# Kernel tuning notes

Hardware: AMD Instinct MI355X
Metric: run time of the kernel (lower is better)

## Reference

```python
import jax, jax.numpy as jnp
import numpy as np

FS, STRIDE, PAD = 3, 1, 1

def setup_inputs() -> dict:
    key = jax.random.key(0)
    k1, k2, k3 = jax.random.split(key, 3)
    N, C, H, W = 4, 256, 64, 64
    out_C = 256
    x = jax.random.normal(k1, (N, C, H, W), jnp.float32)
    # offset/mask conv params (original inits to 0 -> degenerate; use small random)
    offset_w = jax.random.normal(k2, (FS * FS * 3, C, FS, FS), jnp.float32) * 0.01
    offset_b = jnp.zeros((FS * FS * 3,), jnp.float32)
    # xavier_normal-like scale for dcn weight
    dcn_w = jax.random.normal(k3, (out_C, C, FS, FS), jnp.float32) * (1.0 / np.sqrt(C * FS * FS))
    return {"x": x, "offset_w": offset_w, "offset_b": offset_b, "dcn_w": dcn_w}

def _dcnv2(x, offset_w, offset_b, dcn_w):
    fs, stride, pad = FS, STRIDE, PAD
    N, C, H, W = x.shape
    out_C = dcn_w.shape[0]
    K2 = fs * fs
    om = jax.lax.conv_general_dilated(
        x, offset_w, (stride, stride), [(pad, pad), (pad, pad)],
        dimension_numbers=("NCHW", "OIHW", "NCHW")) + offset_b[None, :, None, None]
    Ho, Wo = om.shape[2], om.shape[3]
    offset = om[:, : 2 * K2].reshape(N, K2, 2, Ho, Wo)
    off_y, off_x = offset[:, :, 0], offset[:, :, 1]            # [N,K2,Ho,Wo]
    mask = jax.nn.sigmoid(om[:, 2 * K2:])                      # [N,K2,Ho,Wo]
    # base sampling grid: ori + kernel tap offset
    ky, kx = jnp.meshgrid(jnp.arange(fs), jnp.arange(fs), indexing="ij")
    ky = ky.reshape(K2).astype(jnp.float32)
    kx = kx.reshape(K2).astype(jnp.float32)
    base_y = (jnp.arange(Ho, dtype=jnp.float32) * stride - pad)[None, :, None] + ky[:, None, None]
    base_x = (jnp.arange(Wo, dtype=jnp.float32) * stride - pad)[None, None, :] + kx[:, None, None]
    h_im = base_y[None] + off_y                                # [N,K2,Ho,Wo]
    w_im = base_x[None] + off_x
    y0 = jnp.floor(h_im)
    x0 = jnp.floor(w_im)
    lh, lw = h_im - y0, w_im - x0
    xf = x.reshape(N, C, H * W)

    def gather(yi, xi):
        valid = (yi >= 0) & (yi <= H - 1) & (xi >= 0) & (xi <= W - 1)
        yc = jnp.clip(yi, 0, H - 1).astype(jnp.int32)
        xc = jnp.clip(xi, 0, W - 1).astype(jnp.int32)
        idx = (yc * W + xc).reshape(N, -1)
        v = jax.vmap(lambda img, ind: img[:, ind])(xf, idx)    # [N,C,K2*Ho*Wo]
        v = v.reshape(N, C, K2, Ho, Wo)
        return v * valid[:, None].astype(x.dtype)

    hh, hw = 1.0 - lh, 1.0 - lw
    sampled = ((hh * hw)[:, None] * gather(y0, x0)
               + (hh * lw)[:, None] * gather(y0, x0 + 1)
               + (lh * hw)[:, None] * gather(y0 + 1, x0)
               + (lh * lw)[:, None] * gather(y0 + 1, x0 + 1))  # [N,C,K2,Ho,Wo]
    sampled = sampled * mask[:, None]
    wk = dcn_w.reshape(out_C, C, K2)
    return jnp.einsum("nckhw,ock->nohw", sampled, wk)

def reference(x, offset_w, offset_b, dcn_w):
    return _dcnv2(x, offset_w, offset_b, dcn_w)
```

## Files before the change

### kernel.cpp

```cpp
#include <hip/hip_runtime.h>
#include <hip/hip_bf16.h>
#include <math.h>

#define NB     4
#define CIN    256
#define HH     64
#define WW     64
#define OUTC   256
#define K2     9
#define KTOT   2304
#define HWSZ   4096
#define NSTEPS 72
#define MTOT   16384


typedef __attribute__((ext_vector_type(4)))  float  floatx4;
typedef __attribute__((ext_vector_type(16))) float  floatx16;
typedef __attribute__((ext_vector_type(8)))  short  short8;
typedef __attribute__((ext_vector_type(4)))  short  short4v;
typedef __attribute__((ext_vector_type(4)))  int    intx4;

__device__ __forceinline__ unsigned short f2bf(float f) {
  union { float f; unsigned u; } v; v.f = f;
  unsigned r = v.u + 0x7FFF + ((v.u >> 16) & 1);
  return (unsigned short)(r >> 16);
}
__device__ __forceinline__ float b2f(unsigned short s) {
  union { unsigned u; float f; } v; v.u = ((unsigned)s) << 16;
  return v.f;
}

#define LDS_BARRIER() asm volatile("s_waitcnt lgkmcnt(0)\n\ts_barrier" ::: "memory")

#define WSM_BFRAG   0
#define WSM_B2FRAG  1179648
#define WSM_XT      (1179648 + 147456)
#define WSM_END     (WSM_XT + NB * HWSZ * CIN * 2)
#define WSF_BW      0
#define WSF_B2W     (KTOT * OUTC * 2)
#define WSF_OM      (WSF_B2W + KTOT * 32 * 2)
#define WSF_END     (WSF_OM + NB * 27 * HWSZ * 4)

__global__ __launch_bounds__(256) void prep_main_kernel(
    const float* __restrict__ dcn_w, const float* __restrict__ offw,
    const float* __restrict__ x,
    unsigned short* __restrict__ Bfrag, unsigned short* __restrict__ B2frag,
    unsigned short* __restrict__ xt) {
  int bid = blockIdx.x;
  int tid = threadIdx.x;
  if (bid < 256) {
    __shared__ unsigned short T[64 * 266];
    int img = bid >> 6, h = bid & 63;
    const float* xp = x + (size_t)img * CIN * HWSZ + h * 64;
    int w = tid & 63, cq = tid >> 6;
    for (int cb = 0; cb < 256; cb += 4) {
      int c = cb + cq;
      T[w * 266 + c] = f2bf(xp[(size_t)c * HWSZ + w]);
    }
    __syncthreads();
    int w2 = tid >> 2, cg = (tid & 3) << 6;
    unsigned short* o = xt + ((size_t)(img * 64 + h) * 64 + w2) * 256 + cg;
#pragma unroll
    for (int i = 0; i < 64; i += 8) {
      short8 v = *(short8*)&T[w2 * 266 + cg + i];
      *(short8*)(o + i) = v;
    }
  } else if (bid < 544) {
    int e = (bid - 256) * 256 + tid;
    int lane = e & 63, nt = (e >> 6) & 7, s16 = e >> 9;
    int n = nt * 32 + (lane & 31);
    int kb = s16 * 16 + ((lane >> 5) << 3);
    short8 pk;
#pragma unroll
    for (int j = 0; j < 8; ++j) {
      int k = kb + j;
      pk[j] = (short)f2bf(dcn_w[n * KTOT + (k & 255) * 9 + (k >> 8)]);
    }
    *(short8*)(Bfrag + (size_t)e * 8) = pk;
  } else {
    int e = (bid - 544) * 256 + tid;
    int lane = e & 63, nt = (e >> 6) & 1, s32 = e >> 7;
    int n = nt * 16 + (lane & 15);
    int kb = s32 * 32 + ((lane >> 4) << 3);
    short8 pk;
#pragma unroll
    for (int j = 0; j < 8; ++j) {
      int k = kb + j;
      pk[j] = (n < 27) ? (short)f2bf(offw[n * KTOT + (k & 255) * 9 + (k >> 8)])
                       : (short)0;
    }
    *(short8*)(B2frag + (size_t)e * 8) = pk;
  }
}

__global__ __launch_bounds__(512, 2) void dcn_fused_kernel(
    const unsigned short* __restrict__ xt,
    const unsigned short* __restrict__ Bfrag,
    const unsigned short* __restrict__ B2frag,
    const float* __restrict__ ob, float* __restrict__ out) {
  __shared__ unsigned short Ald[2][520 * 8];
  __shared__ intx4  sOff[576];
  __shared__ float4 sWt[576];
  __shared__ float  omp[4 * 32 * 68];

  int bid = blockIdx.x;
  int img = bid >> 6, h = bid & 63;
  const unsigned short* xb = xt + (size_t)img * HWSZ * 256;

  int tid  = threadIdx.x;
  int lane = tid & 63, q = tid >> 6;
  int quad = lane >> 4, l15 = lane & 15;
  int l31  = lane & 31,  lh5 = lane >> 5;

  if (q < 4) {
    floatx4 cacc[4][2];
#pragma unroll
    for (int mt = 0; mt < 4; ++mt)
#pragma unroll
      for (int nt = 0; nt < 2; ++nt) cacc[mt][nt] = (floatx4){0.f, 0.f, 0.f, 0.f};
    short8 cpa[2][4];
    short8 cpb[2][2];

#define CONV_LOAD(I, SLOT)                                                     \
  {                                                                            \
    int s = q + (I) * 4;                                                       \
    int t = s >> 3;                                                            \
    int dy = t / 3 - 1, dx = t % 3 - 1;                                        \
    int y = h + dy;                                                            \
    int cb0 = ((s & 7) << 5) + (quad << 3);                                    \
    _Pragma("unroll")                                                          \
    for (int mt = 0; mt < 4; ++mt) {                                           \
      int xx = mt * 16 + l15 + dx;                                             \
      short8 v = {0, 0, 0, 0, 0, 0, 0, 0};                                     \
      if (((unsigned)y < 64u) && ((unsigned)xx < 64u))                         \
        v = *(const short8*)(xb + ((y * 64 + xx) << 8) + cb0);                 \
      cpa[SLOT][mt] = v;                                                       \
    }                                                                          \
    _Pragma("unroll")                                                          \
    for (int nt = 0; nt < 2; ++nt)                                             \
      cpb[SLOT][nt] = *(const short8*)(B2frag + (((s * 2 + nt) * 64 + lane) << 3)); \
  }

    CONV_LOAD(0, 0);
#pragma unroll 2
    for (int i = 0; i < 18; ++i) {
      int sl = i & 1;
      if (i < 17) CONV_LOAD(i + 1, sl ^ 1);
#pragma unroll
      for (int mt = 0; mt < 4; ++mt)
#pragma unroll
        for (int nt = 0; nt < 2; ++nt)
          cacc[mt][nt] = __builtin_amdgcn_mfma_f32_16x16x32_bf16(
              cpa[sl][mt], cpb[sl][nt], cacc[mt][nt], 0, 0, 0);
    }
#undef CONV_LOAD
#pragma unroll
    for (int mt = 0; mt < 4; ++mt)
#pragma unroll
      for (int nt = 0; nt < 2; ++nt) {
        int oc = nt * 16 + l15;
        float4 vv = make_float4(cacc[mt][nt][0], cacc[mt][nt][1],
                                cacc[mt][nt][2], cacc[mt][nt][3]);
        *(float4*)&omp[(q * 32 + oc) * 68 + mt * 16 + quad * 4] = vv;
      }
  }
  __syncthreads();

  for (int v = tid; v < 576; v += 512) {
    int w = v & 63, t = v >> 6;
    int ky = t / 3, kx = t % 3;
    float offy = omp[(0 * 32 + 2 * t) * 68 + w] + omp[(1 * 32 + 2 * t) * 68 + w] +
                 omp[(2 * 32 + 2 * t) * 68 + w] + omp[(3 * 32 + 2 * t) * 68 + w] +
                 ob[2 * t];
    float offx = omp[(0 * 32 + 2 * t + 1) * 68 + w] + omp[(1 * 32 + 2 * t + 1) * 68 + w] +
                 omp[(2 * 32 + 2 * t + 1) * 68 + w] + omp[(3 * 32 + 2 * t + 1) * 68 + w] +
                 ob[2 * t + 1];
    float mraw = omp[(0 * 32 + 18 + t) * 68 + w] + omp[(1 * 32 + 18 + t) * 68 + w] +
                 omp[(2 * 32 + 18 + t) * 68 + w] + omp[(3 * 32 + 18 + t) * 68 + w] +
                 ob[18 + t];
    float mv   = 1.0f / (1.0f + __expf(-mraw));
    float him  = (float)(h - 1 + ky) + offy;
    float wim  = (float)(w - 1 + kx) + offx;
    float y0f = floorf(him), x0f = floorf(wim);
    float lhf = him - y0f, lwf = wim - x0f;
    int y0 = (int)y0f, x0i = (int)x0f;
    bool vy0 = (y0 >= 0) && (y0 < HH);
    bool vy1 = (y0 + 1 >= 0) && (y0 + 1 < HH);
    bool vx0 = (x0i >= 0) && (x0i < WW);
    bool vx1 = (x0i + 1 >= 0) && (x0i + 1 < WW);
    float hh_ = 1.0f - lhf, hw_ = 1.0f - lwf;
    float4 wt;
    wt.x = (vy0 && vx0) ? hh_ * hw_ * mv : 0.0f;
    wt.y = (vy0 && vx1) ? hh_ * lwf * mv : 0.0f;
    wt.z = (vy1 && vx0) ? lhf * hw_ * mv : 0.0f;
    wt.w = (vy1 && vx1) ? lhf * lwf * mv : 0.0f;
    int y0c = min(max(y0, 0), 63), y1c = min(max(y0 + 1, 0), 63);
    int x0c = min(max(x0i, 0), 63), x1c = min(max(x0i + 1, 0), 63);
    intx4 ii = {(y0c * 64 + x0c) << 8, (y0c * 64 + x1c) << 8,
                (y1c * 64 + x0c) << 8, (y1c * 64 + x1c) << 8};
    sOff[v] = ii;
    sWt[v]  = wt;
  }

  floatx16 acc[2];
#pragma unroll
  for (int mt = 0; mt < 2; ++mt)
#pragma unroll
    for (int e = 0; e < 16; ++e) acc[mt][e] = 0.f;

  int sm  = tid >> 3;
  int chk = tid & 7;
  int wgran = (((chk >> 1) << 1) + (sm >> 5)) * 65 + ((chk & 1) << 5) + (sm & 31);

  short8 bfr[2][4];
  short8 cr[4];
  float4 pwt;

  __syncthreads();

#pragma unroll
  for (int sub = 0; sub < 4; ++sub)
    bfr[0][sub] = *(const short8*)(
        Bfrag + (((size_t)sub * 8 + q) * 64 + lane) * 8);
  {
    intx4 off = sOff[sm];
    float4 w0 = sWt[sm];
    int cb = chk * 8;
    cr[0] = *(const short8*)(xb + off.x + cb);
    cr[1] = *(const short8*)(xb + off.y + cb);
    cr[2] = *(const short8*)(xb + off.z + cb);
    cr[3] = *(const short8*)(xb + off.w + cb);
    short8 pk;
#pragma unroll
    for (int j = 0; j < 8; ++j) {
      float v = w0.x * b2f((unsigned short)cr[0][j]) +
                w0.y * b2f((unsigned short)cr[1][j]) +
                w0.z * b2f((unsigned short)cr[2][j]) +
                w0.w * b2f((unsigned short)cr[3][j]);
      pk[j] = (short)f2bf(v);
    }
    *(short8*)&Ald[0][wgran * 8] = pk;
  }
  {
    intx4 off = sOff[sm];
    pwt = sWt[sm];
    int cb = 64 + chk * 8;
    cr[0] = *(const short8*)(xb + off.x + cb);
    cr[1] = *(const short8*)(xb + off.y + cb);
    cr[2] = *(const short8*)(xb + off.z + cb);
    cr[3] = *(const short8*)(xb + off.w + cb);
  }
  LDS_BARRIER();

#pragma unroll 2
  for (int s = 0; s < 36; ++s) {
    int cur = s & 1;
    if (s < 35) {
      int s16b = (s + 1) * 4;
#pragma unroll
      for (int sub = 0; sub < 4; ++sub)
        bfr[cur ^ 1][sub] = *(const short8*)(
            Bfrag + (((size_t)(s16b + sub) * 8 + q) * 64 + lane) * 8);
      short8 pk;
#pragma unroll
      for (int j = 0; j < 8; ++j) {
        float v = pwt.x * b2f((unsigned short)cr[0][j]) +
                  pwt.y * b2f((unsigned short)cr[1][j]) +
                  pwt.z * b2f((unsigned short)cr[2][j]) +
                  pwt.w * b2f((unsigned short)cr[3][j]);
        pk[j] = (short)f2bf(v);
      }
      *(short8*)&Ald[cur ^ 1][wgran * 8] = pk;
    }
    if (s < 34) {
      int s2 = s + 2;
      int t2 = s2 >> 2;
      intx4 off = sOff[t2 * 64 + sm];
      pwt = sWt[t2 * 64 + sm];
      int cb = (s2 & 3) * 64 + chk * 8;
      cr[0] = *(const short8*)(xb + off.x + cb);
      cr[1] = *(const short8*)(xb + off.y + cb);
      cr[2] = *(const short8*)(xb + off.z + cb);
      cr[3] = *(const short8*)(xb + off.w + cb);
    }
#pragma unroll
    for (int sub = 0; sub < 4; ++sub) {
      short8 a0 = *(short8*)&Ald[cur][((sub * 2 + 0) * 65 + lane) * 8];
      short8 a1 = *(short8*)&Ald[cur][((sub * 2 + 1) * 65 + lane) * 8];
      acc[0] = __builtin_amdgcn_mfma_f32_32x32x16_bf16(
          a0, bfr[cur][sub], acc[0], 0, 0, 0);
      acc[1] = __builtin_amdgcn_mfma_f32_32x32x16_bf16(
          a1, bfr[cur][sub], acc[1], 0, 0, 0);
    }
    LDS_BARRIER();
  }

  int oc = q * 32 + l31;
#pragma unroll
  for (int mt = 0; mt < 2; ++mt) {
    float* obase = out + (((size_t)img * OUTC + oc) << 12) + h * 64 +
                   mt * 32 + lh5 * 4;
#pragma unroll
    for (int rg = 0; rg < 4; ++rg) {
      float4 vv = make_float4(acc[mt][rg * 4 + 0], acc[mt][rg * 4 + 1],
                              acc[mt][rg * 4 + 2], acc[mt][rg * 4 + 3]);
      *(float4*)(obase + rg * 8) = vv;
    }
  }
}

__global__ __launch_bounds__(256) void prep_fb_kernel(
    const float* __restrict__ dcn_w, const float* __restrict__ offw,
    unsigned short* __restrict__ Bw, unsigned short* __restrict__ B2w) {
  int oc = blockIdx.x;
  for (int k = threadIdx.x; k < KTOT; k += 256) {
    int t = k >> 8, c = k & 255;
    Bw[oc * KTOT + k] = f2bf(dcn_w[oc * KTOT + c * 9 + t]);
    if (oc < 32)
      B2w[oc * KTOT + k] = (oc < 27) ? f2bf(offw[oc * KTOT + c * 9 + t])
                                     : (unsigned short)0;
  }
}

__global__ __launch_bounds__(256) void conv_offset_kernel(
    const float* __restrict__ x, const unsigned short* __restrict__ B2w,
    const float* __restrict__ ob, float* __restrict__ om) {
  __shared__ unsigned short A_lds[64 * 40];
  __shared__ unsigned short B_lds[32 * 40];
  int bid = blockIdx.x;
  int n = bid >> 6, h = bid & 63;
  int tid = threadIdx.x, lane = tid & 63, q = tid >> 6;
  const float* xn = x + n * (CIN * HWSZ);
  floatx4 acc0 = {0.f, 0.f, 0.f, 0.f}, acc1 = {0.f, 0.f, 0.f, 0.f};
  int w = tid & 63, cg = tid >> 6, ocb = tid >> 3, part = tid & 7;
  for (int s = 0; s < NSTEPS; ++s) {
    int t = s >> 3, c0 = (s & 7) << 5;
    int dy = t / 3 - 1, dx = t % 3 - 1;
    __syncthreads();
    {
      int y = h + dy, xx = w + dx;
      bool inb = ((unsigned)y < 64u) && ((unsigned)xx < 64u);
      const float* xb = xn + (c0 + cg * 8) * HWSZ + y * 64 + xx;
      short8 pk;
#pragma unroll
      for (int j = 0; j < 8; ++j) { float v = inb ? xb[j * HWSZ] : 0.0f; pk[j] = (short)f2bf(v); }
      *(short8*)&A_lds[w * 40 + cg * 8] = pk;
    }
    { const unsigned short* bp = B2w + ocb * KTOT + (t << 8) + c0 + part * 4;
      *(short4v*)&B_lds[ocb * 40 + part * 4] = *(const short4v*)bp; }
    __syncthreads();
    int fr = (lane >> 4) * 8;
    short8 af  = *(short8*)&A_lds[(q * 16 + (lane & 15)) * 40 + fr];
    short8 bf0 = *(short8*)&B_lds[((lane & 15)) * 40 + fr];
    short8 bf1 = *(short8*)&B_lds[(16 + (lane & 15)) * 40 + fr];
    acc0 = __builtin_amdgcn_mfma_f32_16x16x32_bf16(af, bf0, acc0, 0, 0, 0);
    acc1 = __builtin_amdgcn_mfma_f32_16x16x32_bf16(af, bf1, acc1, 0, 0, 0);
  }
  int g = lane >> 4;
#pragma unroll
  for (int nt = 0; nt < 2; ++nt) {
    floatx4 a = nt ? acc1 : acc0;
    int oc = nt * 16 + (lane & 15);
    if (oc < 27) {
      float bias = ob[oc];
#pragma unroll
      for (int r = 0; r < 4; ++r) {
        int wm = q * 16 + g * 4 + r;
        float val = a[r] + bias;
        if (oc >= 18) val = 1.0f / (1.0f + __expf(-val));
        om[((n * 27 + oc) << 12) + h * 64 + wm] = val;
      }
    }
  }
}

__global__ __launch_bounds__(256) void dcn_main_kernel(
    const float* __restrict__ x, const float* __restrict__ om,
    const unsigned short* __restrict__ Bw, float* __restrict__ out) {
  __shared__ unsigned short A_lds[32 * 40];
  __shared__ unsigned short B_lds[256 * 40];
  __shared__ int    sY[288];
  __shared__ int    sX[288];
  __shared__ float4 sW[288];
  int bid = blockIdx.x;
  int n = bid >> 7, rem = bid & 127, h = rem >> 1, w0 = (rem & 1) << 5;
  int tid = threadIdx.x, lane = tid & 63, q = tid >> 6;
  const float* xn  = x + n * (CIN * HWSZ);
  const float* omn = om + n * (27 * HWSZ);
  for (int v = tid; v < 288; v += 256) {
    int m = v & 31, t = v >> 5;
    int ky = t / 3, kx = t % 3;
    int wg = w0 + m, sp = h * 64 + wg;
    float offy = omn[(2 * t) * HWSZ + sp];
    float offx = omn[(2 * t + 1) * HWSZ + sp];
    float mv   = omn[(18 + t) * HWSZ + sp];
    float him = (float)(h - 1 + ky) + offy;
    float wim = (float)(wg - 1 + kx) + offx;
    float y0f = floorf(him), x0f = floorf(wim);
    float lh = him - y0f, lw = wim - x0f;
    int y0 = (int)y0f, x0i = (int)x0f;
    bool vy0 = (y0 >= 0) && (y0 < HH), vy1 = (y0 + 1 >= 0) && (y0 + 1 < HH);
    bool vx0 = (x0i >= 0) && (x0i < WW), vx1 = (x0i + 1 >= 0) && (x0i + 1 < WW);
    float hh_ = 1.0f - lh, hw_ = 1.0f - lw;
    float4 wt;
    wt.x = (vy0 && vx0) ? hh_ * hw_ * mv : 0.0f;
    wt.y = (vy0 && vx1) ? hh_ * lw  * mv : 0.0f;
    wt.z = (vy1 && vx0) ? lh  * hw_ * mv : 0.0f;
    wt.w = (vy1 && vx1) ? lh  * lw  * mv : 0.0f;
    sY[v] = y0; sX[v] = x0i; sW[v] = wt;
  }
  floatx4 acc[2][4];
#pragma unroll
  for (int mi = 0; mi < 2; ++mi)
#pragma unroll
    for (int nj = 0; nj < 4; ++nj) acc[mi][nj] = (floatx4){0.f, 0.f, 0.f, 0.f};
  int m = tid & 31, cg = tid >> 5, n0 = q * 64;
  for (int s = 0; s < NSTEPS; ++s) {
    int t = s >> 3, c0 = (s & 7) << 5;
    __syncthreads();
    {
      int p = t * 32 + m;
      int y0 = sY[p], x0i = sX[p];
      float4 wt = sW[p];
      int y0c = min(max(y0, 0), 63), y1c = min(max(y0 + 1, 0), 63);
      int x0c = min(max(x0i, 0), 63), x1c = min(max(x0i + 1, 0), 63);
      int i00 = y0c * 64 + x0c, i01 = y0c * 64 + x1c;
      int i10 = y1c * 64 + x0c, i11 = y1c * 64 + x1c;
      const float* xb = xn + (c0 + cg * 4) * HWSZ;
      short4v pk;
#pragma unroll
      for (int j = 0; j < 4; ++j) {
        const float* xc = xb + j * HWSZ;
        float v = wt.x * xc[i00] + wt.y * xc[i01] + wt.z * xc[i10] + wt.w * xc[i11];
        pk[j] = (short)f2bf(v);
      }
      *(short4v*)&A_lds[m * 40 + cg * 4] = pk;
    }
    {
      const short8* bp = (const short8*)(Bw + tid * KTOT + (t << 8) + c0);
      short8 b0 = bp[0], b1 = bp[1], b2 = bp[2], b3 = bp[3];
      short8* dst = (short8*)&B_lds[tid * 40];
      dst[0] = b0; dst[1] = b1; dst[2] = b2; dst[3] = b3;
    }
    __syncthreads();
    int fr = (lane >> 4) * 8;
    short8 a0 = *(short8*)&A_lds[((lane & 15)) * 40 + fr];
    short8 a1 = *(short8*)&A_lds[(16 + (lane & 15)) * 40 + fr];
#pragma unroll
    for (int nj = 0; nj < 4; ++nj) {
      short8 bfp = *(short8*)&B_lds[(n0 + nj * 16 + (lane & 15)) * 40 + fr];
      acc[0][nj] = __builtin_amdgcn_mfma_f32_16x16x32_bf16(a0, bfp, acc[0][nj], 0, 0, 0);
      acc[1][nj] = __builtin_amdgcn_mfma_f32_16x16x32_bf16(a1, bfp, acc[1][nj], 0, 0, 0);
    }
  }
  int g = lane >> 4;
#pragma unroll
  for (int mi = 0; mi < 2; ++mi) {
    int wm = w0 + mi * 16 + g * 4;
#pragma unroll
    for (int nj = 0; nj < 4; ++nj) {
      int oc = n0 + nj * 16 + (lane & 15);
      float4 vv = make_float4(acc[mi][nj][0], acc[mi][nj][1],
                              acc[mi][nj][2], acc[mi][nj][3]);
      *(float4*)&out[((n * OUTC + oc) << 12) + h * 64 + wm] = vv;
    }
  }
}

extern "C" void kernel_launch(void* const* d_in, const int* in_sizes, int n_in,
                              void* d_out, int out_size, void* d_ws, size_t ws_size,
                              hipStream_t stream) {
  const float* x     = (const float*)d_in[0];
  const float* offw  = (const float*)d_in[1];
  const float* ob    = (const float*)d_in[2];
  const float* dcn_w = (const float*)d_in[3];
  float* out = (float*)d_out;

  if (ws_size >= (size_t)WSM_END) {
    unsigned short* Bfrag  = (unsigned short*)((char*)d_ws + WSM_BFRAG);
    unsigned short* B2frag = (unsigned short*)((char*)d_ws + WSM_B2FRAG);
    unsigned short* xtb    = (unsigned short*)((char*)d_ws + WSM_XT);
    prep_main_kernel<<<580, 256, 0, stream>>>(dcn_w, offw, x, Bfrag, B2frag, xtb);
    dcn_fused_kernel<<<256, 512, 0, stream>>>(xtb, Bfrag, B2frag, ob, out);
  } else {
    unsigned short* Bw  = (unsigned short*)((char*)d_ws + WSF_BW);
    unsigned short* B2w = (unsigned short*)((char*)d_ws + WSF_B2W);
    float*          omb = (float*)((char*)d_ws + WSF_OM);
    prep_fb_kernel<<<256, 256, 0, stream>>>(dcn_w, offw, Bw, B2w);
    conv_offset_kernel<<<NB * HH, 256, 0, stream>>>(x, B2w, ob, omb);
    dcn_main_kernel<<<NB * HH * 2, 256, 0, stream>>>(x, omb, Bw, out);
  }
}
```

Baseline: 126.3 us.

## Deepen gather prefetch to three stages and remap blocks for XCD locality

Double-buffers the bilinear-gather registers so global loads for the im2col tile are issued three steps ahead instead of two, hiding more gather latency behind MFMA work. Also remaps block IDs so that blocks landing on the same XCD process adjacent rows of the same image, improving L2 reuse of the shared input neighborhood. The extra register buffers raise VGPR pressure under the 512-thread, 2-block launch bound and may cause spills.

```diff
diff --git a/kernel.cpp b/kernel.cpp
--- a/kernel.cpp
+++ b/kernel.cpp
@@ -103,7 +103,8 @@
   __shared__ float4 sWt[576];
   __shared__ float  omp[4 * 32 * 68];
 
-  int bid = blockIdx.x;
+  int braw = blockIdx.x;
+  int bid  = ((braw & 7) << 5) + (braw >> 3);
   int img = bid >> 6, h = bid & 63;
   const unsigned short* xb = xt + (size_t)img * HWSZ * 256;
 
@@ -213,8 +214,8 @@
   int wgran = (((chk >> 1) << 1) + (sm >> 5)) * 65 + ((chk & 1) << 5) + (sm & 31);
 
   short8 bfr[2][4];
-  short8 cr[4];
-  float4 pwt;
+  short8 cr[2][4];
+  float4 pwt[2];
 
   __syncthreads();
 
@@ -226,29 +227,35 @@
     intx4 off = sOff[sm];
     float4 w0 = sWt[sm];
     int cb = chk * 8;
-    cr[0] = *(const short8*)(xb + off.x + cb);
-    cr[1] = *(const short8*)(xb + off.y + cb);
-    cr[2] = *(const short8*)(xb + off.z + cb);
-    cr[3] = *(const short8*)(xb + off.w + cb);
+    short8 c0 = *(const short8*)(xb + off.x + cb);
+    short8 c1 = *(const short8*)(xb + off.y + cb);
+    short8 c2 = *(const short8*)(xb + off.z + cb);
+    short8 c3 = *(const short8*)(xb + off.w + cb);
     short8 pk;
 #pragma unroll
     for (int j = 0; j < 8; ++j) {
-      float v = w0.x * b2f((unsigned short)cr[0][j]) +
-                w0.y * b2f((unsigned short)cr[1][j]) +
-                w0.z * b2f((unsigned short)cr[2][j]) +
-                w0.w * b2f((unsigned short)cr[3][j]);
+      float v = w0.x * b2f((unsigned short)c0[j]) +
+                w0.y * b2f((unsigned short)c1[j]) +
+                w0.z * b2f((unsigned short)c2[j]) +
+                w0.w * b2f((unsigned short)c3[j]);
       pk[j] = (short)f2bf(v);
     }
     *(short8*)&Ald[0][wgran * 8] = pk;
   }
   {
     intx4 off = sOff[sm];
-    pwt = sWt[sm];
+    pwt[1] = sWt[sm];
     int cb = 64 + chk * 8;
-    cr[0] = *(const short8*)(xb + off.x + cb);
-    cr[1] = *(const short8*)(xb + off.y + cb);
-    cr[2] = *(const short8*)(xb + off.z + cb);
-    cr[3] = *(const short8*)(xb + off.w + cb);
+    cr[1][0] = *(const short8*)(xb + off.x + cb);
+    cr[1][1] = *(const short8*)(xb + off.y + cb);
+    cr[1][2] = *(const short8*)(xb + off.z + cb);
+    cr[1][3] = *(const short8*)(xb + off.w + cb);
+    pwt[0] = sWt[sm];
+    int cb2 = 128 + chk * 8;
+    cr[0][0] = *(const short8*)(xb + off.x + cb2);
+    cr[0][1] = *(const short8*)(xb + off.y + cb2);
+    cr[0][2] = *(const short8*)(xb + off.z + cb2);
+    cr[0][3] = *(const short8*)(xb + off.w + cb2);
   }
   LDS_BARRIER();
 
@@ -261,27 +268,28 @@
       for (int sub = 0; sub < 4; ++sub)
         bfr[cur ^ 1][sub] = *(const short8*)(
             Bfrag + (((size_t)(s16b + sub) * 8 + q) * 64 + lane) * 8);
+      float4 w = pwt[cur ^ 1];
       short8 pk;
 #pragma unroll
       for (int j = 0; j < 8; ++j) {
-        float v = pwt.x * b2f((unsigned short)cr[0][j]) +
-                  pwt.y * b2f((unsigned short)cr[1][j]) +
-                  pwt.z * b2f((unsigned short)cr[2][j]) +
-                  pwt.w * b2f((unsigned short)cr[3][j]);
+        float v = w.x * b2f((unsigned short)cr[cur ^ 1][0][j]) +
+                  w.y * b2f((unsigned short)cr[cur ^ 1][1][j]) +
+                  w.z * b2f((unsigned short)cr[cur ^ 1][2][j]) +
+                  w.w * b2f((unsigned short)cr[cur ^ 1][3][j]);
         pk[j] = (short)f2bf(v);
       }
       *(short8*)&Ald[cur ^ 1][wgran * 8] = pk;
     }
-    if (s < 34) {
-      int s2 = s + 2;
-      int t2 = s2 >> 2;
-      intx4 off = sOff[t2 * 64 + sm];
-      pwt = sWt[t2 * 64 + sm];
-      int cb = (s2 & 3) * 64 + chk * 8;
-      cr[0] = *(const short8*)(xb + off.x + cb);
-      cr[1] = *(const short8*)(xb + off.y + cb);
-      cr[2] = *(const short8*)(xb + off.z + cb);
-      cr[3] = *(const short8*)(xb + off.w + cb);
+    if (s < 33) {
+      int s3 = s + 3;
+      int t3 = s3 >> 2;
+      intx4 off = sOff[t3 * 64 + sm];
+      pwt[cur ^ 1] = sWt[t3 * 64 + sm];
+      int cb = (s3 & 3) * 64 + chk * 8;
+      cr[cur ^ 1][0] = *(const short8*)(xb + off.x + cb);
+      cr[cur ^ 1][1] = *(const short8*)(xb + off.y + cb);
+      cr[cur ^ 1][2] = *(const short8*)(xb + off.z + cb);
+      cr[cur ^ 1][3] = *(const short8*)(xb + off.w + cb);
     }
 #pragma unroll
     for (int sub = 0; sub < 4; ++sub) {
```

Result: no change. 124.9 us (-1.1%).

## Restructure DCN main loop into per-tap groups with deeper LDS buffering and packed bf16 conversion

Applied to the files above, without the earlier changes.

Reorganizes the 36-step K loop into 9 groups, each covering one kernel tap across all 256 channels. Each group issues 16 bilinear corner loads per thread at once, packs the interpolated values with v_cvt_pk_bf16_f32, and uses an 8-slot LDS ring, so barriers drop from 36 to 9. It also remaps block IDs to interleave images and rows, and raises wave priority around the MFMA section. The cost is much higher register pressure (16 B-fragments and 16 corner vectors held live) and 4x the LDS for the A tile, which may cut occupancy under the 512x2 launch bound.

```diff
diff --git a/kernel.cpp b/kernel.cpp
--- a/kernel.cpp
+++ b/kernel.cpp
@@ -28,6 +28,32 @@
 __device__ __forceinline__ float b2f(unsigned short s) {
   union { unsigned u; float f; } v; v.u = ((unsigned)s) << 16;
   return v.f;
+}
+__device__ __forceinline__ float lo16f(int u) {
+  union { int i; float f; } v; v.i = u << 16; return v.f;
+}
+__device__ __forceinline__ float hi16f(int u) {
+  union { int i; float f; } v; v.i = u & 0xFFFF0000; return v.f;
+}
+__device__ __forceinline__ unsigned cvt_pk_bf16(float lo, float hi) {
+  unsigned r;
+  asm("v_cvt_pk_bf16_f32 %0, %1, %2" : "=v"(r) : "v"(lo), "v"(hi));
+  return r;
+}
+
+__device__ __forceinline__ void pack8(const intx4& c0, const intx4& c1,
+                                      const intx4& c2, const intx4& c3,
+                                      const float4& w, unsigned short* dst) {
+  intx4 o;
+#pragma unroll
+  for (int jj = 0; jj < 4; ++jj) {
+    float v0 = w.x * lo16f(c0[jj]) + w.y * lo16f(c1[jj]) +
+               w.z * lo16f(c2[jj]) + w.w * lo16f(c3[jj]);
+    float v1 = w.x * hi16f(c0[jj]) + w.y * hi16f(c1[jj]) +
+               w.z * hi16f(c2[jj]) + w.w * hi16f(c3[jj]);
+    o[jj] = (int)cvt_pk_bf16(v0, v1);
+  }
+  *(intx4*)dst = o;
 }
 
 #define LDS_BARRIER() asm volatile("s_waitcnt lgkmcnt(0)\n\ts_barrier" ::: "memory")
@@ -98,12 +124,13 @@
     const unsigned short* __restrict__ Bfrag,
     const unsigned short* __restrict__ B2frag,
     const float* __restrict__ ob, float* __restrict__ out) {
-  __shared__ unsigned short Ald[2][520 * 8];
+  __shared__ unsigned short Ald[8][520 * 8];
   __shared__ intx4  sOff[576];
   __shared__ float4 sWt[576];
   __shared__ float  omp[4 * 32 * 68];
 
-  int bid = blockIdx.x;
+  int braw = blockIdx.x;
+  int bid  = ((braw & 7) << 5) + (braw >> 3);
   int img = bid >> 6, h = bid & 63;
   const unsigned short* xb = xt + (size_t)img * HWSZ * 256;
 
@@ -212,86 +239,91 @@
   int chk = tid & 7;
   int wgran = (((chk >> 1) << 1) + (sm >> 5)) * 65 + ((chk & 1) << 5) + (sm & 31);
 
-  short8 bfr[2][4];
-  short8 cr[4];
-  float4 pwt;
+  short8 bfr[4][4];
+  intx4  cr[4][4];
+  float4 pwtA, pwtN;
 
   __syncthreads();
 
 #pragma unroll
-  for (int sub = 0; sub < 4; ++sub)
-    bfr[0][sub] = *(const short8*)(
-        Bfrag + (((size_t)sub * 8 + q) * 64 + lane) * 8);
+  for (int u = 0; u < 4; ++u)
+#pragma unroll
+    for (int sub = 0; sub < 4; ++sub)
+      bfr[u][sub] = *(const short8*)(
+          Bfrag + (((size_t)(u * 4 + sub) * 8 + q) * 64 + lane) * 8);
   {
-    intx4 off = sOff[sm];
+    intx4 off0 = sOff[sm];
     float4 w0 = sWt[sm];
-    int cb = chk * 8;
-    cr[0] = *(const short8*)(xb + off.x + cb);
-    cr[1] = *(const short8*)(xb + off.y + cb);
-    cr[2] = *(const short8*)(xb + off.z + cb);
-    cr[3] = *(const short8*)(xb + off.w + cb);
-    short8 pk;
-#pragma unroll
-    for (int j = 0; j < 8; ++j) {
-      float v = w0.x * b2f((unsigned short)cr[0][j]) +
-                w0.y * b2f((unsigned short)cr[1][j]) +
-                w0.z * b2f((unsigned short)cr[2][j]) +
-                w0.w * b2f((unsigned short)cr[3][j]);
-      pk[j] = (short)f2bf(v);
-    }
-    *(short8*)&Ald[0][wgran * 8] = pk;
-  }
-  {
-    intx4 off = sOff[sm];
-    pwt = sWt[sm];
-    int cb = 64 + chk * 8;
-    cr[0] = *(const short8*)(xb + off.x + cb);
-    cr[1] = *(const short8*)(xb + off.y + cb);
-    cr[2] = *(const short8*)(xb + off.z + cb);
-    cr[3] = *(const short8*)(xb + off.w + cb);
+#pragma unroll
+    for (int u = 0; u < 4; ++u) {
+      int cb = u * 64 + chk * 8;
+      intx4 c0 = *(const intx4*)(xb + off0.x + cb);
+      intx4 c1 = *(const intx4*)(xb + off0.y + cb);
+      intx4 c2 = *(const intx4*)(xb + off0.z + cb);
+      intx4 c3 = *(const intx4*)(xb + off0.w + cb);
+      pack8(c0, c1, c2, c3, w0, &Ald[u][wgran * 8]);
+    }
+    intx4 off1 = sOff[64 + sm];
+    pwtA = sWt[64 + sm];
+    pwtN = pwtA;
+#pragma unroll
+    for (int u = 0; u < 4; ++u) {
+      int cb = u * 64 + chk * 8;
+      cr[u][0] = *(const intx4*)(xb + off1.x + cb);
+      cr[u][1] = *(const intx4*)(xb + off1.y + cb);
+      cr[u][2] = *(const intx4*)(xb + off1.z + cb);
+      cr[u][3] = *(const intx4*)(xb + off1.w + cb);
+    }
   }
   LDS_BARRIER();
 
-#pragma unroll 2
-  for (int s = 0; s < 36; ++s) {
-    int cur = s & 1;
-    if (s < 35) {
-      int s16b = (s + 1) * 4;
-#pragma unroll
-      for (int sub = 0; sub < 4; ++sub)
-        bfr[cur ^ 1][sub] = *(const short8*)(
-            Bfrag + (((size_t)(s16b + sub) * 8 + q) * 64 + lane) * 8);
-      short8 pk;
-#pragma unroll
-      for (int j = 0; j < 8; ++j) {
-        float v = pwt.x * b2f((unsigned short)cr[0][j]) +
-                  pwt.y * b2f((unsigned short)cr[1][j]) +
-                  pwt.z * b2f((unsigned short)cr[2][j]) +
-                  pwt.w * b2f((unsigned short)cr[3][j]);
-        pk[j] = (short)f2bf(v);
+#pragma unroll 1
+  for (int G = 0; G < 9; ++G) {
+    int s0 = 4 * G;
+    if (G < 8) {
+#pragma unroll
+      for (int u = 0; u < 4; ++u)
+        pack8(cr[u][0], cr[u][1], cr[u][2], cr[u][3], pwtA,
+              &Ald[(s0 + 4 + u) & 7][wgran * 8]);
+    }
+    if (G < 7) {
+      intx4 offN = sOff[(G + 2) * 64 + sm];
+      pwtN = sWt[(G + 2) * 64 + sm];
+#pragma unroll
+      for (int u = 0; u < 4; ++u) {
+        int cb = u * 64 + chk * 8;
+        cr[u][0] = *(const intx4*)(xb + offN.x + cb);
+        cr[u][1] = *(const intx4*)(xb + offN.y + cb);
+        cr[u][2] = *(const intx4*)(xb + offN.z + cb);
+        cr[u][3] = *(const intx4*)(xb + offN.w + cb);
       }
-      *(short8*)&Ald[cur ^ 1][wgran * 8] = pk;
-    }
-    if (s < 34) {
-      int s2 = s + 2;
-      int t2 = s2 >> 2;
-      intx4 off = sOff[t2 * 64 + sm];
-      pwt = sWt[t2 * 64 + sm];
-      int cb = (s2 & 3) * 64 + chk * 8;
-      cr[0] = *(const short8*)(xb + off.x + cb);
-      cr[1] = *(const short8*)(xb + off.y + cb);
-      cr[2] = *(const short8*)(xb + off.z + cb);
-      cr[3] = *(const short8*)(xb + off.w + cb);
-    }
-#pragma unroll
-    for (int sub = 0; sub < 4; ++sub) {
-      short8 a0 = *(short8*)&Ald[cur][((sub * 2 + 0) * 65 + lane) * 8];
-      short8 a1 = *(short8*)&Ald[cur][((sub * 2 + 1) * 65 + lane) * 8];
-      acc[0] = __builtin_amdgcn_mfma_f32_32x32x16_bf16(
-          a0, bfr[cur][sub], acc[0], 0, 0, 0);
-      acc[1] = __builtin_amdgcn_mfma_f32_32x32x16_bf16(
-          a1, bfr[cur][sub], acc[1], 0, 0, 0);
-    }
+    }
+    __builtin_amdgcn_s_setprio(1);
+#pragma unroll
+    for (int u = 0; u < 4; ++u) {
+      const unsigned short* Ab = Ald[(s0 + u) & 7];
+#pragma unroll
+      for (int sub = 0; sub < 4; ++sub) {
+        short8 a0 = *(short8*)&Ab[((sub * 2 + 0) * 65 + lane) * 8];
+        short8 a1 = *(short8*)&Ab[((sub * 2 + 1) * 65 + lane) * 8];
+        acc[0] = __builtin_amdgcn_mfma_f32_32x32x16_bf16(
+            a0, bfr[u][sub], acc[0], 0, 0, 0);
+        acc[1] = __builtin_amdgcn_mfma_f32_32x32x16_bf16(
+            a1, bfr[u][sub], acc[1], 0, 0, 0);
+      }
+    }
+    __builtin_amdgcn_s_setprio(0);
+    if (G < 8) {
+#pragma unroll
+      for (int u = 0; u < 4; ++u) {
+        int s16b = (s0 + 4 + u) * 4;
+#pragma unroll
+        for (int sub = 0; sub < 4; ++sub)
+          bfr[u][sub] = *(const short8*)(
+              Bfrag + (((size_t)(s16b + sub) * 8 + q) * 64 + lane) * 8);
+      }
+    }
+    pwtA = pwtN;
     LDS_BARRIER();
   }
 
```

Result: faster. 122.8 us (-2.8%).
